# Optimization experiments

Measured on AMD Instinct MI355X. Metric: run time of the kernel, lower is better.

The kernel has to match this reference:

```python
import jax, jax.numpy as jnp
import numpy as np

MD_R = 64          # low-rank R
NMF_STEPS = 7      # EVAL_STEPS
INV_T = 1.0
EPS = 1e-6
GN_GROUPS = 32


def _nmf_step(x, bases, coef):
    # x: (B,D,N), bases: (B,D,R), coef: (B,N,R) -- multiplicative NMF updates
    btb = jnp.einsum('bdr,bdk->brk', bases, bases)                 # (B,R,R)
    coef = coef * jnp.einsum('bdn,bdr->bnr', x, bases) / (
        jnp.einsum('bnr,brk->bnk', coef, btb) + EPS)
    ctc = jnp.einsum('bnr,bnk->brk', coef, coef)                   # (B,R,R)
    bases = bases * jnp.einsum('bdn,bnr->bdr', x, coef) / (
        jnp.einsum('bdr,brk->bdk', bases, ctc) + EPS)
    return bases, coef


def setup_inputs() -> dict:
    key = jax.random.key(0)
    ks = jax.random.split(key, 7)
    B, C, H, W = 8, 256, 64, 64
    x = jax.random.normal(ks[0], (B, C, H, W), jnp.float32)
    w_in = jax.random.normal(ks[1], (C, C), jnp.float32) * 0.02
    b_in = jnp.zeros((C,), jnp.float32)
    w_out = jax.random.normal(ks[2], (C, C), jnp.float32) * 0.02
    gn_gamma = jnp.ones((C,), jnp.float32)
    gn_beta = jnp.zeros((C,), jnp.float32)
    bases_init = jax.random.uniform(ks[3], (B, C, MD_R), jnp.float32)  # RAND_INIT bases
    return {"x": x, "w_in": w_in, "b_in": b_in, "w_out": w_out,
            "gn_gamma": gn_gamma, "gn_beta": gn_beta, "bases_init": bases_init}


def reference(x, w_in, b_in, w_out, gn_gamma, gn_beta, bases_init):
    B, C, H, W = x.shape
    N = H * W
    # ham_in: 1x1 conv with bias, then relu
    h = jnp.einsum('bchw,oc->bohw', x, w_in) + b_in[None, :, None, None]
    h = jax.nn.relu(h)
    # NMF2D: flatten spatial (SPATIAL=True, S=1 -> D=C)
    xm = h.reshape(B, C, N)                                         # (B,D,N)
    # F.normalize(rand bases, dim=1)
    bases = bases_init / jnp.maximum(
        jnp.linalg.norm(bases_init, axis=1, keepdims=True), 1e-12)
    # local_inference runs under no_grad in the original; math identical here
    xs = jax.lax.stop_gradient(xm)
    coef = jax.nn.softmax(INV_T * jnp.einsum('bdn,bdr->bnr', xs, bases), axis=-1)
    for _ in range(NMF_STEPS):
        bases, coef = _nmf_step(xs, bases, coef)
    bases = jax.lax.stop_gradient(bases)
    coef = jax.lax.stop_gradient(coef)
    # compute_coef (differentiable w.r.t. xm)
    btb = jnp.einsum('bdr,bdk->brk', bases, bases)
    coef = coef * jnp.einsum('bdn,bdr->bnr', xm, bases) / (
        jnp.einsum('bnr,brk->bnk', coef, btb) + EPS)
    rec = jnp.einsum('bdr,bnr->bdn', bases, coef).reshape(B, C, H, W)
    # ham_out: 1x1 conv (no bias) + GroupNorm(32)
    o = jnp.einsum('bchw,oc->bohw', rec, w_out)
    g = o.reshape(B, GN_GROUPS, C // GN_GROUPS, H, W)
    mu = g.mean(axis=(2, 3, 4), keepdims=True)
    var = g.var(axis=(2, 3, 4), keepdims=True)
    g = (g - mu) * jax.lax.rsqrt(var + 1e-5)
    o = g.reshape(B, C, H, W) * gn_gamma[None, :, None, None] + gn_beta[None, :, None, None]
    # residual + relu
    return jax.nn.relu(x + o)
```

## Files before the change

kernel.cpp:

```cpp
#include <hip/hip_runtime.h>

#define B_ 8
#define C_ 256
#define N_ 4096
#define R_ 64
#define STEPS_ 7
#define NCH_ 128
#define NSP_ 32
#define EPS_ 1e-6f

typedef unsigned short u16;
typedef short bf8v __attribute__((ext_vector_type(8)));
typedef float f4v __attribute__((ext_vector_type(4)));

#define MFMA(a, b, c) __builtin_amdgcn_mfma_f32_16x16x32_bf16((a), (b), (c), 0, 0, 0)

__device__ __forceinline__ u16 bf(float x) {
  union { float f; unsigned u; } v; v.f = x;
  return (u16)((v.u + 0x7FFFu + ((v.u >> 16) & 1u)) >> 16);
}
__device__ __forceinline__ float bf2f(u16 x) {
  union { unsigned u; float f; } v; v.u = (unsigned)x << 16; return v.f;
}
__device__ __forceinline__ bf8v ldf(const u16* p) { return *(const bf8v*)p; }

__global__ __launch_bounds__(256)
void prep_kernel(const float* __restrict__ binit, float* __restrict__ bases,
                 u16* __restrict__ bases_bf, u16* __restrict__ basesT,
                 const float* __restrict__ w1, const float* __restrict__ w2,
                 u16* __restrict__ w1b, u16* __restrict__ w2b) {
  const int t = threadIdx.x;
  if (blockIdx.x >= 8) {
    const int i = (blockIdx.x - 8) * 256 + t;
    w1b[i] = bf(w1[i]);
    w2b[i] = bf(w2[i]);
    return;
  }
  const int b = blockIdx.x;
  const int rr = t & 63, dq = t >> 6;
  const float* src = binit + (size_t)b * C_ * R_;
  float* dst = bases + (size_t)b * C_ * R_;
  u16* dbf = bases_bf + (size_t)b * C_ * R_;
  u16* dT  = basesT + (size_t)b * R_ * C_;
  float vals[64];
  float s = 0.f;
#pragma unroll
  for (int i = 0; i < 64; ++i) {
    float v = src[(size_t)(dq + 4 * i) * R_ + rr];
    vals[i] = v; s = fmaf(v, v, s);
  }
  __shared__ float red[4][64];
  red[dq][rr] = s;
  __syncthreads();
  float nrm = fmaxf(sqrtf(red[0][rr] + red[1][rr] + red[2][rr] + red[3][rr]), 1e-12f);
  const float inv = 1.f / nrm;
#pragma unroll
  for (int i = 0; i < 64; ++i) {
    const int d = dq + 4 * i;
    const float v = vals[i] * inv;
    dst[(size_t)d * R_ + rr] = v;
    dbf[(size_t)d * R_ + rr] = bf(v);
    dT[(size_t)rr * C_ + d]  = bf(v);
  }
}

__global__ __launch_bounds__(256)
void xpose_kernel(const float* __restrict__ x, u16* __restrict__ xT) {
  const int n0 = blockIdx.x * 64, c0 = blockIdx.y * 64, b = blockIdx.z;
  __shared__ float lds[64][65];
  const int t = threadIdx.x;
  const float* xb = x + (size_t)b * C_ * N_;
  const int row = t >> 4, col4 = (t & 15) * 4;
#pragma unroll
  for (int p = 0; p < 4; ++p) {
    float4 v = *(const float4*)&xb[(size_t)(c0 + row + 16 * p) * N_ + n0 + col4];
    lds[row + 16 * p][col4 + 0] = v.x; lds[row + 16 * p][col4 + 1] = v.y;
    lds[row + 16 * p][col4 + 2] = v.z; lds[row + 16 * p][col4 + 3] = v.w;
  }
  __syncthreads();
  const int r = t >> 2, cb = (t & 3) * 16;
  __align__(16) u16 tmp[16];
#pragma unroll
  for (int j = 0; j < 16; ++j) tmp[j] = bf(lds[cb + j][r]);
  u16* o = xT + (size_t)b * N_ * C_ + (size_t)(n0 + r) * C_ + c0 + cb;
  *(uint4*)o = *(uint4*)tmp;
  *(uint4*)(o + 8) = *(uint4*)(tmp + 8);
}

template<bool CONV1>
__global__ __launch_bounds__(256)
void conv_mfma_kernel(const u16* __restrict__ A, const u16* __restrict__ W,
                      const float* __restrict__ bias, u16* __restrict__ h_dn,
                      u16* __restrict__ h_nd, float* __restrict__ of32,
                      float* __restrict__ pstats) {
  const int nb0 = blockIdx.x * 128, ob0 = blockIdx.y * 128, b = blockIdx.z;
  const int t = threadIdx.x, w = t >> 6, lane = t & 63, g = lane >> 4, c = lane & 15;
  const int n_base = nb0 + (w >> 1) * 64, o_base = ob0 + (w & 1) * 64;
  const u16* Ab = A + (size_t)b * N_ * C_;
  f4v acc[4][4] = {};
  for (int k0 = 0; k0 < C_; k0 += 32) {
    bf8v av[4], wv[4];
#pragma unroll
    for (int mi = 0; mi < 4; ++mi)
      av[mi] = ldf(Ab + (size_t)(n_base + mi * 16 + c) * C_ + k0 + g * 8);
#pragma unroll
    for (int nj = 0; nj < 4; ++nj)
      wv[nj] = ldf(W + (size_t)(o_base + nj * 16 + c) * C_ + k0 + g * 8);
#pragma unroll
    for (int mi = 0; mi < 4; ++mi)
#pragma unroll
      for (int nj = 0; nj < 4; ++nj)
        acc[mi][nj] = MFMA(av[mi], wv[nj], acc[mi][nj]);
  }
  __shared__ float lds[64][65];
  float sacc0 = 0.f, sacc1 = 0.f, s2acc0 = 0.f, s2acc1 = 0.f;
  for (int p = 0; p < 4; ++p) {
    if (w == p) {
#pragma unroll
      for (int mi = 0; mi < 4; ++mi)
#pragma unroll
        for (int nj = 0; nj < 4; ++nj) {
          const float bb = CONV1 ? bias[o_base + nj * 16 + c] : 0.f;
#pragma unroll
          for (int rg = 0; rg < 4; ++rg) {
            float v = acc[mi][nj][rg];
            if (CONV1) v = fmaxf(v + bb, 0.f);
            lds[mi * 16 + g * 4 + rg][nj * 16 + c] = v;
          }
        }
    }
    __syncthreads();
    const int pn = nb0 + (p >> 1) * 64, po = ob0 + (p & 1) * 64;
    if (CONV1) {
      {
        const int n = t >> 2, ob2 = (t & 3) * 16;
        __align__(16) u16 tmp[16];
#pragma unroll
        for (int j = 0; j < 16; ++j) tmp[j] = bf(lds[n][ob2 + j]);
        u16* o = h_nd + (size_t)b * N_ * C_ + (size_t)(pn + n) * C_ + po + ob2;
        *(uint4*)o = *(uint4*)tmp; *(uint4*)(o + 8) = *(uint4*)(tmp + 8);
      }
      {
        const int oo = t >> 2, nb2 = (t & 3) * 16;
        __align__(16) u16 tmp[16];
#pragma unroll
        for (int j = 0; j < 16; ++j) tmp[j] = bf(lds[nb2 + j][oo]);
        u16* o = h_dn + (size_t)b * C_ * N_ + (size_t)(po + oo) * N_ + pn + nb2;
        *(uint4*)o = *(uint4*)tmp; *(uint4*)(o + 8) = *(uint4*)(tmp + 8);
      }
    } else {
      const int oo = t >> 2, nb2 = (t & 3) * 16;
      float* o = of32 + (size_t)b * C_ * N_ + (size_t)(po + oo) * N_ + pn + nb2;
      float ls = 0.f, ls2 = 0.f;
#pragma unroll
      for (int q = 0; q < 4; ++q) {
        float4 v = make_float4(lds[nb2 + q * 4 + 0][oo], lds[nb2 + q * 4 + 1][oo],
                               lds[nb2 + q * 4 + 2][oo], lds[nb2 + q * 4 + 3][oo]);
        *(float4*)&o[q * 4] = v;
        ls += v.x + v.y + v.z + v.w;
        ls2 = fmaf(v.x, v.x, ls2); ls2 = fmaf(v.y, v.y, ls2);
        ls2 = fmaf(v.z, v.z, ls2); ls2 = fmaf(v.w, v.w, ls2);
      }
      if ((p & 1) == 0) { sacc0 += ls; s2acc0 += ls2; }
      else              { sacc1 += ls; s2acc1 += ls2; }
    }
    __syncthreads();
  }
  if (!CONV1) {
    const int oo = t >> 2, q4 = t & 3;
    lds[oo][q4] = sacc0;      lds[oo][4 + q4] = s2acc0;
    lds[oo][8 + q4] = sacc1;  lds[oo][12 + q4] = s2acc1;
    __syncthreads();
    if (t < 128) {
      const int hh = t >> 6, oo2 = t & 63;
      const int base = hh * 8;
      float s = lds[oo2][base] + lds[oo2][base + 1] + lds[oo2][base + 2] + lds[oo2][base + 3];
      float s2 = lds[oo2][base + 4] + lds[oo2][base + 5] + lds[oo2][base + 6] + lds[oo2][base + 7];
      float* ps = pstats + (((size_t)blockIdx.z * 32 + blockIdx.x) * 256 +
                            (size_t)blockIdx.y * 128 + hh * 64 + oo2) * 2;
      ps[0] = s; ps[1] = s2;
    }
  }
}

template<int MODE>
__global__ __launch_bounds__(512)
void nmf_kernel(const u16* __restrict__ h_nd, const u16* __restrict__ h_dn,
                const u16* __restrict__ basesT, const u16* __restrict__ bases_bf,
                u16* __restrict__ coef_bf, u16* __restrict__ rec_nd,
                float* __restrict__ ctcp, float* __restrict__ xcp) {
  const int nc0 = blockIdx.x * NCH_;
  const int b = blockIdx.y;
  const int t = threadIdx.x, w = t >> 6, lane = t & 63, g = lane >> 4, c = lane & 15;
  __shared__ u16 bT_s[64 * 256];
  __shared__ u16 btb_s[64][72];
  __shared__ u16 coef_s[128][72];
  __shared__ u16 coefT_s[64][136];
  const u16* hb = h_nd + (size_t)b * N_ * C_;
  const u16* bT = basesT + (size_t)b * R_ * C_;
  u16* cb = coef_bf + (size_t)b * N_ * R_;

#pragma unroll
  for (int i = 0; i < 4; ++i) {
    const int lin = t + i * 512;
    const int r = lin >> 5, k = lin & 31;
    *(uint4*)&bT_s[r * 256 + ((k ^ (r & 7)) * 8)] =
        *(const uint4*)&bT[(size_t)r * C_ + k * 8];
  }
  if (MODE != 0) {
    const int row = t >> 2, seg = (t & 3) * 16;
    const u16* src = cb + (size_t)(nc0 + row) * R_ + seg;
    *(uint4*)&coef_s[row][seg] = *(const uint4*)src;
    *(uint4*)&coef_s[row][seg + 8] = *(const uint4*)(src + 8);
  }
  __syncthreads();

  const int nl = w * 16 + c;

  f4v num[4] = {}, bt[4] = {};
  const u16* An = hb + (size_t)(nc0 + nl) * C_;
  for (int k0 = 0; k0 < C_; k0 += 32) {
    const int kc = (k0 >> 3) + g;
    bf8v bv[4];
#pragma unroll
    for (int nj = 0; nj < 4; ++nj)
      bv[nj] = *(const bf8v*)&bT_s[(nj * 16 + c) * 256 + ((kc ^ (c & 7)) * 8)];
    bf8v a = ldf(An + k0 + g * 8);
#pragma unroll
    for (int nj = 0; nj < 4; ++nj) num[nj] = MFMA(a, bv[nj], num[nj]);
    if (MODE != 0 && w < 4) {
      bf8v a2 = *(const bf8v*)&bT_s[(w * 16 + c) * 256 + ((kc ^ (c & 7)) * 8)];
#pragma unroll
      for (int nj = 0; nj < 4; ++nj) bt[nj] = MFMA(a2, bv[nj], bt[nj]);
    }
  }

  if (MODE == 0) {
#pragma unroll
    for (int rg = 0; rg < 4; ++rg) {
      float m = fmaxf(fmaxf(num[0][rg], num[1][rg]), fmaxf(num[2][rg], num[3][rg]));
#pragma unroll
      for (int off = 1; off < 16; off <<= 1) m = fmaxf(m, __shfl_xor(m, off));
      float e[4], s = 0.f;
#pragma unroll
      for (int nj = 0; nj < 4; ++nj) { e[nj] = __expf(num[nj][rg] - m); s += e[nj]; }
#pragma unroll
      for (int off = 1; off < 16; off <<= 1) s += __shfl_xor(s, off);
      const float inv = 1.f / s;
      const int n = nc0 + w * 16 + g * 4 + rg;
#pragma unroll
      for (int nj = 0; nj < 4; ++nj)
        cb[(size_t)n * R_ + nj * 16 + c] = bf(e[nj] * inv);
    }
    return;
  }

  if (w < 4) {
#pragma unroll
    for (int nj = 0; nj < 4; ++nj)
#pragma unroll
      for (int rg = 0; rg < 4; ++rg)
        btb_s[w * 16 + g * 4 + rg][nj * 16 + c] = bf(bt[nj][rg]);
  }
  __syncthreads();

  f4v den[4] = {};
#pragma unroll
  for (int k0 = 0; k0 < R_; k0 += 32) {
    bf8v a = *(const bf8v*)&coef_s[nl][k0 + g * 8];
#pragma unroll
    for (int nj = 0; nj < 4; ++nj)
      den[nj] = MFMA(a, *(const bf8v*)&btb_s[nj * 16 + c][k0 + g * 8], den[nj]);
  }
  __syncthreads();

#pragma unroll
  for (int nj = 0; nj < 4; ++nj)
#pragma unroll
    for (int rg = 0; rg < 4; ++rg) {
      const int row = w * 16 + g * 4 + rg, r = nj * 16 + c;
      const float old = bf2f(coef_s[row][r]);
      const u16 nv = bf(old * num[nj][rg] / (den[nj][rg] + EPS_));
      coef_s[row][r] = nv;
      if (MODE == 1) coefT_s[r][row] = nv;
    }
  __syncthreads();

  {
    const int row = t >> 2, seg = (t & 3) * 16;
    u16* dst = cb + (size_t)(nc0 + row) * R_ + seg;
    *(uint4*)dst = *(const uint4*)&coef_s[row][seg];
    *(uint4*)(dst + 8) = *(const uint4*)&coef_s[row][seg + 8];
  }

  if (MODE == 1) {
    f4v xa[2][4] = {};
    const u16* hd = h_dn + (size_t)b * C_ * N_;
    for (int k0 = 0; k0 < NCH_; k0 += 32) {
      bf8v bv[4];
#pragma unroll
      for (int nj = 0; nj < 4; ++nj)
        bv[nj] = *(const bf8v*)&coefT_s[nj * 16 + c][k0 + g * 8];
#pragma unroll
      for (int mi = 0; mi < 2; ++mi) {
        bf8v a = ldf(hd + (size_t)(w * 32 + mi * 16 + c) * N_ + nc0 + k0 + g * 8);
#pragma unroll
        for (int nj = 0; nj < 4; ++nj) xa[mi][nj] = MFMA(a, bv[nj], xa[mi][nj]);
      }
    }
    float* xo = xcp + ((size_t)b * NSP_ + blockIdx.x) * (C_ * R_);
#pragma unroll
    for (int mi = 0; mi < 2; ++mi)
#pragma unroll
      for (int nj = 0; nj < 4; ++nj)
#pragma unroll
        for (int rg = 0; rg < 4; ++rg)
          xo[(size_t)(w * 32 + mi * 16 + g * 4 + rg) * R_ + nj * 16 + c] = xa[mi][nj][rg];
    if (w < 4) {
      f4v ca[4] = {};
      for (int k0 = 0; k0 < NCH_; k0 += 32) {
        bf8v a = *(const bf8v*)&coefT_s[w * 16 + c][k0 + g * 8];
#pragma unroll
        for (int nj = 0; nj < 4; ++nj)
          ca[nj] = MFMA(a, *(const bf8v*)&coefT_s[nj * 16 + c][k0 + g * 8], ca[nj]);
      }
      float* co = ctcp + ((size_t)b * NSP_ + blockIdx.x) * (R_ * R_);
#pragma unroll
      for (int nj = 0; nj < 4; ++nj)
#pragma unroll
        for (int rg = 0; rg < 4; ++rg)
          co[(size_t)(w * 16 + g * 4 + rg) * R_ + nj * 16 + c] = ca[nj][rg];
    }
  }

  if (MODE == 2) {
    f4v ra[8][2] = {};
    const u16* Bb = bases_bf + (size_t)b * C_ * R_;
#pragma unroll
    for (int k0 = 0; k0 < R_; k0 += 32) {
      bf8v bv[2];
#pragma unroll
      for (int nj = 0; nj < 2; ++nj)
        bv[nj] = ldf(Bb + (size_t)(w * 32 + nj * 16 + c) * R_ + k0 + g * 8);
#pragma unroll
      for (int mi = 0; mi < 8; ++mi) {
        bf8v a = *(const bf8v*)&coef_s[mi * 16 + c][k0 + g * 8];
#pragma unroll
        for (int nj = 0; nj < 2; ++nj) ra[mi][nj] = MFMA(a, bv[nj], ra[mi][nj]);
      }
    }
    u16* ro = rec_nd + (size_t)b * N_ * C_;
#pragma unroll
    for (int mi = 0; mi < 8; ++mi)
#pragma unroll
      for (int nj = 0; nj < 2; ++nj)
#pragma unroll
        for (int rg = 0; rg < 4; ++rg)
          ro[(size_t)(nc0 + mi * 16 + g * 4 + rg) * C_ + w * 32 + nj * 16 + c] =
              bf(ra[mi][nj][rg]);
  }
}

__global__ __launch_bounds__(256)
void bases_update_kernel(const float* __restrict__ xcp, const float* __restrict__ ctcp,
                         float* __restrict__ bases, u16* __restrict__ bases_bf,
                         u16* __restrict__ basesT) {
  const int dt = blockIdx.x & 3, rt = blockIdx.x >> 2, b = blockIdx.y;
  const int d0 = dt * 64, rb = rt * 16;
  float* bb = bases + (size_t)b * C_ * R_;
  __shared__ float ctc_s[64][16];
  __shared__ float b_s[64][65];
  const int t = threadIdx.x;
  {
    const int k = t >> 2, cr = (t & 3) * 4;
    float4 a = make_float4(0, 0, 0, 0);
    for (int s = 0; s < NSP_; ++s) {
      float4 v = *(const float4*)&ctcp[((size_t)b * NSP_ + s) * (R_ * R_) + (size_t)k * R_ + rb + cr];
      a.x += v.x; a.y += v.y; a.z += v.z; a.w += v.w;
    }
    *(float4*)&ctc_s[k][cr] = a;
  }
  {
    const int lc = t & 63, lr = t >> 6;
#pragma unroll
    for (int p = 0; p < 16; ++p)
      b_s[lr + 4 * p][lc] = bb[(size_t)(d0 + lr + 4 * p) * R_ + lc];
  }
  __syncthreads();
  const int dd = t >> 2, r0 = rb + (t & 3) * 4, cr = (t & 3) * 4;
  float4 num2 = make_float4(0, 0, 0, 0);
  for (int s = 0; s < NSP_; ++s) {
    float4 v = *(const float4*)&xcp[(((size_t)b * NSP_ + s) * C_ + d0 + dd) * R_ + r0];
    num2.x += v.x; num2.y += v.y; num2.z += v.z; num2.w += v.w;
  }
  float4 den = make_float4(0, 0, 0, 0);
#pragma unroll
  for (int k = 0; k < 64; ++k) {
    const float a = b_s[dd][k];
    float4 cv = *(const float4*)&ctc_s[k][cr];
    den.x = fmaf(a, cv.x, den.x); den.y = fmaf(a, cv.y, den.y);
    den.z = fmaf(a, cv.z, den.z); den.w = fmaf(a, cv.w, den.w);
  }
  float4 o;
  o.x = b_s[dd][r0 + 0] * num2.x / (den.x + EPS_);
  o.y = b_s[dd][r0 + 1] * num2.y / (den.y + EPS_);
  o.z = b_s[dd][r0 + 2] * num2.z / (den.z + EPS_);
  o.w = b_s[dd][r0 + 3] * num2.w / (den.w + EPS_);
  *(float4*)&bb[(size_t)(d0 + dd) * R_ + r0] = o;
  u16* obf = bases_bf + (size_t)b * C_ * R_ + (size_t)(d0 + dd) * R_ + r0;
  obf[0] = bf(o.x); obf[1] = bf(o.y); obf[2] = bf(o.z); obf[3] = bf(o.w);
  u16* oT = basesT + (size_t)b * R_ * C_ + d0 + dd;
  oT[(size_t)(r0 + 0) * C_] = bf(o.x); oT[(size_t)(r0 + 1) * C_] = bf(o.y);
  oT[(size_t)(r0 + 2) * C_] = bf(o.z); oT[(size_t)(r0 + 3) * C_] = bf(o.w);
}

__global__ __launch_bounds__(256)
void gn_final_kernel(const float* __restrict__ x, const float* __restrict__ gamma,
                     const float* __restrict__ beta, const float* __restrict__ pstats,
                     float* __restrict__ out) {
  const int t = threadIdx.x;
  const size_t gid0 = (size_t)blockIdx.x * 256;
  const size_t idx0 = gid0 * 4;
  const int b = (int)(idx0 >> 20);
  const int c = (int)((idx0 & ((1u << 20) - 1)) >> 12);
  const int g = c >> 3;
  float s, s2;
  {
    const int nb = t >> 3, ch = g * 8 + (t & 7);
    const float* ps = pstats + (((size_t)b * 32 + nb) * 256 + ch) * 2;
    s = ps[0]; s2 = ps[1];
  }
#pragma unroll
  for (int off = 32; off > 0; off >>= 1) { s += __shfl_down(s, off); s2 += __shfl_down(s2, off); }
  __shared__ float rs[4], rs2[4], fin[2];
  if ((t & 63) == 0) { rs[t >> 6] = s; rs2[t >> 6] = s2; }
  __syncthreads();
  if (t == 0) {
    float S = rs[0] + rs[1] + rs[2] + rs[3];
    float S2 = rs2[0] + rs2[1] + rs2[2] + rs2[3];
    float mean = S / 32768.f;
    float var = S2 / 32768.f - mean * mean;
    fin[0] = mean; fin[1] = rsqrtf(var + 1e-5f);
  }
  __syncthreads();
  const float mean = fin[0], rstd = fin[1];
  const float ga = gamma[c] * rstd;
  const float be = beta[c] - mean * ga;
  const size_t gid = gid0 + t;
  float4 ov = ((const float4*)out)[gid];
  float4 xv = ((const float4*)x)[gid];
  float4 r;
  r.x = fmaxf(fmaf(ov.x, ga, be) + xv.x, 0.f);
  r.y = fmaxf(fmaf(ov.y, ga, be) + xv.y, 0.f);
  r.z = fmaxf(fmaf(ov.z, ga, be) + xv.z, 0.f);
  r.w = fmaxf(fmaf(ov.w, ga, be) + xv.w, 0.f);
  ((float4*)out)[gid] = r;
}

extern "C" void kernel_launch(void* const* d_in, const int* in_sizes, int n_in,
                              void* d_out, int out_size, void* d_ws, size_t ws_size,
                              hipStream_t stream) {
  (void)in_sizes; (void)n_in; (void)out_size; (void)ws_size;
  const float* x     = (const float*)d_in[0];
  const float* w_in  = (const float*)d_in[1];
  const float* b_in  = (const float*)d_in[2];
  const float* w_out = (const float*)d_in[3];
  const float* gamma = (const float*)d_in[4];
  const float* beta  = (const float*)d_in[5];
  const float* binit = (const float*)d_in[6];
  float* out = (float*)d_out;

  float* p = (float*)d_ws;
  u16* xT = (u16*)p;        p += 4194304;
  u16* rec_nd = xT;
  u16* h_nd = (u16*)p;      p += 4194304;
  u16* h_dn = (u16*)p;      p += 4194304;
  u16* coef_bf = (u16*)p;   p += 1048576;
  float* bases = p;         p += 131072;
  u16* bases_bf = (u16*)p;  p += 65536;
  u16* basesT = (u16*)p;    p += 65536;
  float* ctcp = p;          p += 1048576;
  float* xcp = p;           p += 4194304;
  u16* w1b = (u16*)p;       p += 32768;
  u16* w2b = (u16*)p;       p += 32768;
  float* pstats = p;        p += 131072;

  prep_kernel<<<dim3(264), 256, 0, stream>>>(binit, bases, bases_bf, basesT,
                                             w_in, w_out, w1b, w2b);
  xpose_kernel<<<dim3(64, 4, 8), 256, 0, stream>>>(x, xT);
  conv_mfma_kernel<true><<<dim3(32, 2, 8), 256, 0, stream>>>(xT, w1b, b_in, h_dn, h_nd,
                                                             nullptr, nullptr);
  nmf_kernel<0><<<dim3(32, 8), 512, 0, stream>>>(h_nd, h_dn, basesT, bases_bf, coef_bf,
                                                 nullptr, nullptr, nullptr);
  for (int it = 0; it < STEPS_; ++it) {
    nmf_kernel<1><<<dim3(32, 8), 512, 0, stream>>>(h_nd, h_dn, basesT, bases_bf, coef_bf,
                                                   nullptr, ctcp, xcp);
    bases_update_kernel<<<dim3(16, 8), 256, 0, stream>>>(xcp, ctcp, bases, bases_bf, basesT);
  }
  nmf_kernel<2><<<dim3(32, 8), 512, 0, stream>>>(h_nd, h_dn, basesT, bases_bf, coef_bf,
                                                 rec_nd, nullptr, nullptr);
  conv_mfma_kernel<false><<<dim3(32, 2, 8), 256, 0, stream>>>(rec_nd, w2b, nullptr,
                                                              nullptr, nullptr, out, pstats);
  gn_final_kernel<<<dim3((B_ * C_ * N_) / 4 / 256), 256, 0, stream>>>(x, gamma, beta,
                                                                      pstats, out);
}
```

Baseline: 287.6 us.

## Fold w_out into bases and fuse softmax init into first NMF step

Computes M2 = W_out·bases once per batch (low-rank, C×R) and runs the output conv directly on coef (K=64 instead of K=256), so the rank-R reconstruction tensor is never materialized in global memory. Also merges the softmax initialization pass into the first NMF iteration, which removes one full nmf_kernel launch and one read of h_nd. The bf16 bases copy is dropped. The reassociation changes rounding slightly because M2 is stored in bf16.

```diff
diff --git a/kernel.cpp b/kernel.cpp
--- a/kernel.cpp
+++ b/kernel.cpp
@@ -26,7 +26,7 @@
 
 __global__ __launch_bounds__(256)
 void prep_kernel(const float* __restrict__ binit, float* __restrict__ bases,
-                 u16* __restrict__ bases_bf, u16* __restrict__ basesT,
+                 u16* __restrict__ basesT,
                  const float* __restrict__ w1, const float* __restrict__ w2,
                  u16* __restrict__ w1b, u16* __restrict__ w2b) {
   const int t = threadIdx.x;
@@ -40,7 +40,6 @@
   const int rr = t & 63, dq = t >> 6;
   const float* src = binit + (size_t)b * C_ * R_;
   float* dst = bases + (size_t)b * C_ * R_;
-  u16* dbf = bases_bf + (size_t)b * C_ * R_;
   u16* dT  = basesT + (size_t)b * R_ * C_;
   float vals[64];
   float s = 0.f;
@@ -59,7 +58,6 @@
     const int d = dq + 4 * i;
     const float v = vals[i] * inv;
     dst[(size_t)d * R_ + rr] = v;
-    dbf[(size_t)d * R_ + rr] = bf(v);
     dT[(size_t)rr * C_ + d]  = bf(v);
   }
 }
@@ -87,12 +85,10 @@
   *(uint4*)(o + 8) = *(uint4*)(tmp + 8);
 }
 
-template<bool CONV1>
 __global__ __launch_bounds__(256)
-void conv_mfma_kernel(const u16* __restrict__ A, const u16* __restrict__ W,
-                      const float* __restrict__ bias, u16* __restrict__ h_dn,
-                      u16* __restrict__ h_nd, float* __restrict__ of32,
-                      float* __restrict__ pstats) {
+void conv1_kernel(const u16* __restrict__ A, const u16* __restrict__ W,
+                  const float* __restrict__ bias, u16* __restrict__ h_dn,
+                  u16* __restrict__ h_nd) {
   const int nb0 = blockIdx.x * 128, ob0 = blockIdx.y * 128, b = blockIdx.z;
   const int t = threadIdx.x, w = t >> 6, lane = t & 63, g = lane >> 4, c = lane & 15;
   const int n_base = nb0 + (w >> 1) * 64, o_base = ob0 + (w & 1) * 64;
@@ -113,60 +109,319 @@
         acc[mi][nj] = MFMA(av[mi], wv[nj], acc[mi][nj]);
   }
   __shared__ float lds[64][65];
+  for (int p = 0; p < 4; ++p) {
+    if (w == p) {
+#pragma unroll
+      for (int mi = 0; mi < 4; ++mi)
+#pragma unroll
+        for (int nj = 0; nj < 4; ++nj) {
+          const float bb = bias[o_base + nj * 16 + c];
+#pragma unroll
+          for (int rg = 0; rg < 4; ++rg)
+            lds[mi * 16 + g * 4 + rg][nj * 16 + c] = fmaxf(acc[mi][nj][rg] + bb, 0.f);
+        }
+    }
+    __syncthreads();
+    const int pn = nb0 + (p >> 1) * 64, po = ob0 + (p & 1) * 64;
+    {
+      const int n = t >> 2, ob2 = (t & 3) * 16;
+      __align__(16) u16 tmp[16];
+#pragma unroll
+      for (int j = 0; j < 16; ++j) tmp[j] = bf(lds[n][ob2 + j]);
+      u16* o = h_nd + (size_t)b * N_ * C_ + (size_t)(pn + n) * C_ + po + ob2;
+      *(uint4*)o = *(uint4*)tmp; *(uint4*)(o + 8) = *(uint4*)(tmp + 8);
+    }
+    {
+      const int oo = t >> 2, nb2 = (t & 3) * 16;
+      __align__(16) u16 tmp[16];
+#pragma unroll
+      for (int j = 0; j < 16; ++j) tmp[j] = bf(lds[nb2 + j][oo]);
+      u16* o = h_dn + (size_t)b * C_ * N_ + (size_t)(po + oo) * N_ + pn + nb2;
+      *(uint4*)o = *(uint4*)tmp; *(uint4*)(o + 8) = *(uint4*)(tmp + 8);
+    }
+    __syncthreads();
+  }
+}
+
+template<int MODE>
+__global__ __launch_bounds__(512)
+void nmf_kernel(const u16* __restrict__ h_nd, const u16* __restrict__ h_dn,
+                const u16* __restrict__ basesT, const u16* __restrict__ w2b,
+                u16* __restrict__ coef_bf, u16* __restrict__ m2_bf,
+                float* __restrict__ ctcp, float* __restrict__ xcp) {
+  const int nc0 = blockIdx.x * NCH_;
+  const int b = blockIdx.y;
+  const int t = threadIdx.x, w = t >> 6, lane = t & 63, g = lane >> 4, c = lane & 15;
+  __shared__ u16 bT_s[64 * 256];
+  __shared__ u16 btb_s[64][72];
+  __shared__ u16 coef_s[128][72];
+  __shared__ u16 coefT_s[64][136];
+  const u16* hb = h_nd + (size_t)b * N_ * C_;
+  const u16* bT = basesT + (size_t)b * R_ * C_;
+  u16* cb = coef_bf + (size_t)b * N_ * R_;
+
+#pragma unroll
+  for (int i = 0; i < 4; ++i) {
+    const int lin = t + i * 512;
+    const int r = lin >> 5, k = lin & 31;
+    *(uint4*)&bT_s[r * 256 + ((k ^ (r & 7)) * 8)] =
+        *(const uint4*)&bT[(size_t)r * C_ + k * 8];
+  }
+  if (MODE != 0) {
+    const int row = t >> 2, seg = (t & 3) * 16;
+    const u16* src = cb + (size_t)(nc0 + row) * R_ + seg;
+    *(uint4*)&coef_s[row][seg] = *(const uint4*)src;
+    *(uint4*)&coef_s[row][seg + 8] = *(const uint4*)(src + 8);
+  }
+  __syncthreads();
+
+  const int nl = w * 16 + c;
+
+  f4v num[4] = {}, bt[4] = {};
+  const u16* An = hb + (size_t)(nc0 + nl) * C_;
+  for (int k0 = 0; k0 < C_; k0 += 32) {
+    const int kc = (k0 >> 3) + g;
+    bf8v bv[4];
+#pragma unroll
+    for (int nj = 0; nj < 4; ++nj)
+      bv[nj] = *(const bf8v*)&bT_s[(nj * 16 + c) * 256 + ((kc ^ (c & 7)) * 8)];
+    bf8v a = ldf(An + k0 + g * 8);
+#pragma unroll
+    for (int nj = 0; nj < 4; ++nj) num[nj] = MFMA(a, bv[nj], num[nj]);
+    if (w < 4) {
+      bf8v a2 = *(const bf8v*)&bT_s[(w * 16 + c) * 256 + ((kc ^ (c & 7)) * 8)];
+#pragma unroll
+      for (int nj = 0; nj < 4; ++nj) bt[nj] = MFMA(a2, bv[nj], bt[nj]);
+    }
+  }
+
+  if (MODE == 0) {
+#pragma unroll
+    for (int rg = 0; rg < 4; ++rg) {
+      float m = fmaxf(fmaxf(num[0][rg], num[1][rg]), fmaxf(num[2][rg], num[3][rg]));
+#pragma unroll
+      for (int off = 1; off < 16; off <<= 1) m = fmaxf(m, __shfl_xor(m, off));
+      float e[4], s = 0.f;
+#pragma unroll
+      for (int nj = 0; nj < 4; ++nj) { e[nj] = __expf(num[nj][rg] - m); s += e[nj]; }
+#pragma unroll
+      for (int off = 1; off < 16; off <<= 1) s += __shfl_xor(s, off);
+      const float inv = 1.f / s;
+#pragma unroll
+      for (int nj = 0; nj < 4; ++nj)
+        coef_s[w * 16 + g * 4 + rg][nj * 16 + c] = bf(e[nj] * inv);
+    }
+  }
+
+  if (w < 4) {
+#pragma unroll
+    for (int nj = 0; nj < 4; ++nj)
+#pragma unroll
+      for (int rg = 0; rg < 4; ++rg)
+        btb_s[w * 16 + g * 4 + rg][nj * 16 + c] = bf(bt[nj][rg]);
+  }
+  __syncthreads();
+
+  f4v den[4] = {};
+#pragma unroll
+  for (int k0 = 0; k0 < R_; k0 += 32) {
+    bf8v a = *(const bf8v*)&coef_s[nl][k0 + g * 8];
+#pragma unroll
+    for (int nj = 0; nj < 4; ++nj)
+      den[nj] = MFMA(a, *(const bf8v*)&btb_s[nj * 16 + c][k0 + g * 8], den[nj]);
+  }
+  __syncthreads();
+
+#pragma unroll
+  for (int nj = 0; nj < 4; ++nj)
+#pragma unroll
+    for (int rg = 0; rg < 4; ++rg) {
+      const int row = w * 16 + g * 4 + rg, r = nj * 16 + c;
+      const float old = bf2f(coef_s[row][r]);
+      const u16 nv = bf(old * num[nj][rg] / (den[nj][rg] + EPS_));
+      coef_s[row][r] = nv;
+      if (MODE <= 1) coefT_s[r][row] = nv;
+    }
+  __syncthreads();
+
+  {
+    const int row = t >> 2, seg = (t & 3) * 16;
+    u16* dst = cb + (size_t)(nc0 + row) * R_ + seg;
+    *(uint4*)dst = *(const uint4*)&coef_s[row][seg];
+    *(uint4*)(dst + 8) = *(const uint4*)&coef_s[row][seg + 8];
+  }
+
+  if (MODE <= 1) {
+    f4v xa[2][4] = {};
+    const u16* hd = h_dn + (size_t)b * C_ * N_;
+    for (int k0 = 0; k0 < NCH_; k0 += 32) {
+      bf8v bv[4];
+#pragma unroll
+      for (int nj = 0; nj < 4; ++nj)
+        bv[nj] = *(const bf8v*)&coefT_s[nj * 16 + c][k0 + g * 8];
+#pragma unroll
+      for (int mi = 0; mi < 2; ++mi) {
+        bf8v a = ldf(hd + (size_t)(w * 32 + mi * 16 + c) * N_ + nc0 + k0 + g * 8);
+#pragma unroll
+        for (int nj = 0; nj < 4; ++nj) xa[mi][nj] = MFMA(a, bv[nj], xa[mi][nj]);
+      }
+    }
+    float* xo = xcp + ((size_t)b * NSP_ + blockIdx.x) * (C_ * R_);
+#pragma unroll
+    for (int mi = 0; mi < 2; ++mi)
+#pragma unroll
+      for (int nj = 0; nj < 4; ++nj)
+#pragma unroll
+        for (int rg = 0; rg < 4; ++rg)
+          xo[(size_t)(w * 32 + mi * 16 + g * 4 + rg) * R_ + nj * 16 + c] = xa[mi][nj][rg];
+    if (w < 4) {
+      f4v ca[4] = {};
+      for (int k0 = 0; k0 < NCH_; k0 += 32) {
+        bf8v a = *(const bf8v*)&coefT_s[w * 16 + c][k0 + g * 8];
+#pragma unroll
+        for (int nj = 0; nj < 4; ++nj)
+          ca[nj] = MFMA(a, *(const bf8v*)&coefT_s[nj * 16 + c][k0 + g * 8], ca[nj]);
+      }
+      float* co = ctcp + ((size_t)b * NSP_ + blockIdx.x) * (R_ * R_);
+#pragma unroll
+      for (int nj = 0; nj < 4; ++nj)
+#pragma unroll
+        for (int rg = 0; rg < 4; ++rg)
+          co[(size_t)(w * 16 + g * 4 + rg) * R_ + nj * 16 + c] = ca[nj][rg];
+    }
+  }
+
+  if (MODE == 2 && blockIdx.x == 0) {
+    f4v ma[2][4] = {};
+    for (int k0 = 0; k0 < C_; k0 += 32) {
+      const int kc = (k0 >> 3) + g;
+      bf8v bv[4];
+#pragma unroll
+      for (int nj = 0; nj < 4; ++nj)
+        bv[nj] = *(const bf8v*)&bT_s[(nj * 16 + c) * 256 + ((kc ^ (c & 7)) * 8)];
+#pragma unroll
+      for (int mi = 0; mi < 2; ++mi) {
+        bf8v a = ldf(w2b + (size_t)(w * 32 + mi * 16 + c) * C_ + k0 + g * 8);
+#pragma unroll
+        for (int nj = 0; nj < 4; ++nj) ma[mi][nj] = MFMA(a, bv[nj], ma[mi][nj]);
+      }
+    }
+    u16* mo = m2_bf + (size_t)b * C_ * R_;
+#pragma unroll
+    for (int mi = 0; mi < 2; ++mi)
+#pragma unroll
+      for (int nj = 0; nj < 4; ++nj)
+#pragma unroll
+        for (int rg = 0; rg < 4; ++rg)
+          mo[(size_t)(w * 32 + mi * 16 + g * 4 + rg) * R_ + nj * 16 + c] = bf(ma[mi][nj][rg]);
+  }
+}
+
+__global__ __launch_bounds__(256)
+void bases_update_kernel(const float* __restrict__ xcp, const float* __restrict__ ctcp,
+                         float* __restrict__ bases, u16* __restrict__ basesT) {
+  const int dt = blockIdx.x & 3, rt = blockIdx.x >> 2, b = blockIdx.y;
+  const int d0 = dt * 64, rb = rt * 16;
+  float* bb = bases + (size_t)b * C_ * R_;
+  __shared__ float ctc_s[64][16];
+  __shared__ float b_s[64][65];
+  const int t = threadIdx.x;
+  {
+    const int k = t >> 2, cr = (t & 3) * 4;
+    float4 a = make_float4(0, 0, 0, 0);
+    for (int s = 0; s < NSP_; ++s) {
+      float4 v = *(const float4*)&ctcp[((size_t)b * NSP_ + s) * (R_ * R_) + (size_t)k * R_ + rb + cr];
+      a.x += v.x; a.y += v.y; a.z += v.z; a.w += v.w;
+    }
+    *(float4*)&ctc_s[k][cr] = a;
+  }
+  {
+    const int lc = t & 63, lr = t >> 6;
+#pragma unroll
+    for (int p = 0; p < 16; ++p)
+      b_s[lr + 4 * p][lc] = bb[(size_t)(d0 + lr + 4 * p) * R_ + lc];
+  }
+  __syncthreads();
+  const int dd = t >> 2, r0 = rb + (t & 3) * 4, cr = (t & 3) * 4;
+  float4 num2 = make_float4(0, 0, 0, 0);
+  for (int s = 0; s < NSP_; ++s) {
+    float4 v = *(const float4*)&xcp[(((size_t)b * NSP_ + s) * C_ + d0 + dd) * R_ + r0];
+    num2.x += v.x; num2.y += v.y; num2.z += v.z; num2.w += v.w;
+  }
+  float4 den = make_float4(0, 0, 0, 0);
+#pragma unroll
+  for (int k = 0; k < 64; ++k) {
+    const float a = b_s[dd][k];
+    float4 cv = *(const float4*)&ctc_s[k][cr];
+    den.x = fmaf(a, cv.x, den.x); den.y = fmaf(a, cv.y, den.y);
+    den.z = fmaf(a, cv.z, den.z); den.w = fmaf(a, cv.w, den.w);
+  }
+  float4 o;
+  o.x = b_s[dd][r0 + 0] * num2.x / (den.x + EPS_);
+  o.y = b_s[dd][r0 + 1] * num2.y / (den.y + EPS_);
+  o.z = b_s[dd][r0 + 2] * num2.z / (den.z + EPS_);
+  o.w = b_s[dd][r0 + 3] * num2.w / (den.w + EPS_);
+  *(float4*)&bb[(size_t)(d0 + dd) * R_ + r0] = o;
+  u16* oT = basesT + (size_t)b * R_ * C_ + d0 + dd;
+  oT[(size_t)(r0 + 0) * C_] = bf(o.x); oT[(size_t)(r0 + 1) * C_] = bf(o.y);
+  oT[(size_t)(r0 + 2) * C_] = bf(o.z); oT[(size_t)(r0 + 3) * C_] = bf(o.w);
+}
+
+__global__ __launch_bounds__(256)
+void conv2_kernel(const u16* __restrict__ coef, const u16* __restrict__ m2,
+                  float* __restrict__ of32, float* __restrict__ pstats) {
+  const int nb0 = blockIdx.x * 128, ob0 = blockIdx.y * 128, b = blockIdx.z;
+  const int t = threadIdx.x, w = t >> 6, lane = t & 63, g = lane >> 4, c = lane & 15;
+  const int n_base = nb0 + (w >> 1) * 64, o_base = ob0 + (w & 1) * 64;
+  const u16* Ab = coef + (size_t)b * N_ * R_;
+  const u16* Wb = m2 + (size_t)b * C_ * R_;
+  f4v acc[4][4] = {};
+#pragma unroll
+  for (int k0 = 0; k0 < R_; k0 += 32) {
+    bf8v av[4], wv[4];
+#pragma unroll
+    for (int mi = 0; mi < 4; ++mi)
+      av[mi] = ldf(Ab + (size_t)(n_base + mi * 16 + c) * R_ + k0 + g * 8);
+#pragma unroll
+    for (int nj = 0; nj < 4; ++nj)
+      wv[nj] = ldf(Wb + (size_t)(o_base + nj * 16 + c) * R_ + k0 + g * 8);
+#pragma unroll
+    for (int mi = 0; mi < 4; ++mi)
+#pragma unroll
+      for (int nj = 0; nj < 4; ++nj)
+        acc[mi][nj] = MFMA(av[mi], wv[nj], acc[mi][nj]);
+  }
+  __shared__ float lds[64][65];
   float sacc0 = 0.f, sacc1 = 0.f, s2acc0 = 0.f, s2acc1 = 0.f;
   for (int p = 0; p < 4; ++p) {
     if (w == p) {
 #pragma unroll
       for (int mi = 0; mi < 4; ++mi)
 #pragma unroll
-        for (int nj = 0; nj < 4; ++nj) {
-          const float bb = CONV1 ? bias[o_base + nj * 16 + c] : 0.f;
-#pragma unroll
-          for (int rg = 0; rg < 4; ++rg) {
-            float v = acc[mi][nj][rg];
-            if (CONV1) v = fmaxf(v + bb, 0.f);
-            lds[mi * 16 + g * 4 + rg][nj * 16 + c] = v;
-          }
-        }
+        for (int nj = 0; nj < 4; ++nj)
+#pragma unroll
+          for (int rg = 0; rg < 4; ++rg)
+            lds[mi * 16 + g * 4 + rg][nj * 16 + c] = acc[mi][nj][rg];
     }
     __syncthreads();
     const int pn = nb0 + (p >> 1) * 64, po = ob0 + (p & 1) * 64;
-    if (CONV1) {
-      {
-        const int n = t >> 2, ob2 = (t & 3) * 16;
-        __align__(16) u16 tmp[16];
-#pragma unroll
-        for (int j = 0; j < 16; ++j) tmp[j] = bf(lds[n][ob2 + j]);
-        u16* o = h_nd + (size_t)b * N_ * C_ + (size_t)(pn + n) * C_ + po + ob2;
-        *(uint4*)o = *(uint4*)tmp; *(uint4*)(o + 8) = *(uint4*)(tmp + 8);
-      }
-      {
-        const int oo = t >> 2, nb2 = (t & 3) * 16;
-        __align__(16) u16 tmp[16];
-#pragma unroll
-        for (int j = 0; j < 16; ++j) tmp[j] = bf(lds[nb2 + j][oo]);
-        u16* o = h_dn + (size_t)b * C_ * N_ + (size_t)(po + oo) * N_ + pn + nb2;
-        *(uint4*)o = *(uint4*)tmp; *(uint4*)(o + 8) = *(uint4*)(tmp + 8);
-      }
-    } else {
-      const int oo = t >> 2, nb2 = (t & 3) * 16;
-      float* o = of32 + (size_t)b * C_ * N_ + (size_t)(po + oo) * N_ + pn + nb2;
-      float ls = 0.f, ls2 = 0.f;
-#pragma unroll
-      for (int q = 0; q < 4; ++q) {
-        float4 v = make_float4(lds[nb2 + q * 4 + 0][oo], lds[nb2 + q * 4 + 1][oo],
-                               lds[nb2 + q * 4 + 2][oo], lds[nb2 + q * 4 + 3][oo]);
-        *(float4*)&o[q * 4] = v;
-        ls += v.x + v.y + v.z + v.w;
-        ls2 = fmaf(v.x, v.x, ls2); ls2 = fmaf(v.y, v.y, ls2);
-        ls2 = fmaf(v.z, v.z, ls2); ls2 = fmaf(v.w, v.w, ls2);
-      }
-      if ((p & 1) == 0) { sacc0 += ls; s2acc0 += ls2; }
-      else              { sacc1 += ls; s2acc1 += ls2; }
-    }
+    const int oo = t >> 2, nb2 = (t & 3) * 16;
+    float* o = of32 + (size_t)b * C_ * N_ + (size_t)(po + oo) * N_ + pn + nb2;
+    float ls = 0.f, ls2 = 0.f;
+#pragma unroll
+    for (int q = 0; q < 4; ++q) {
+      float4 v = make_float4(lds[nb2 + q * 4 + 0][oo], lds[nb2 + q * 4 + 1][oo],
+                             lds[nb2 + q * 4 + 2][oo], lds[nb2 + q * 4 + 3][oo]);
+      *(float4*)&o[q * 4] = v;
+      ls += v.x + v.y + v.z + v.w;
+      ls2 = fmaf(v.x, v.x, ls2); ls2 = fmaf(v.y, v.y, ls2);
+      ls2 = fmaf(v.z, v.z, ls2); ls2 = fmaf(v.w, v.w, ls2);
+    }
+    if ((p & 1) == 0) { sacc0 += ls; s2acc0 += ls2; }
+    else              { sacc1 += ls; s2acc1 += ls2; }
     __syncthreads();
   }
-  if (!CONV1) {
+  {
     const int oo = t >> 2, q4 = t & 3;
     lds[oo][q4] = sacc0;      lds[oo][4 + q4] = s2acc0;
     lds[oo][8 + q4] = sacc1;  lds[oo][12 + q4] = s2acc1;
@@ -181,237 +436,6 @@
       ps[0] = s; ps[1] = s2;
     }
   }
-}
-
-template<int MODE>
-__global__ __launch_bounds__(512)
-void nmf_kernel(const u16* __restrict__ h_nd, const u16* __restrict__ h_dn,
-                const u16* __restrict__ basesT, const u16* __restrict__ bases_bf,
-                u16* __restrict__ coef_bf, u16* __restrict__ rec_nd,
-                float* __restrict__ ctcp, float* __restrict__ xcp) {
-  const int nc0 = blockIdx.x * NCH_;
-  const int b = blockIdx.y;
-  const int t = threadIdx.x, w = t >> 6, lane = t & 63, g = lane >> 4, c = lane & 15;
-  __shared__ u16 bT_s[64 * 256];
-  __shared__ u16 btb_s[64][72];
-  __shared__ u16 coef_s[128][72];
-  __shared__ u16 coefT_s[64][136];
-  const u16* hb = h_nd + (size_t)b * N_ * C_;
-  const u16* bT = basesT + (size_t)b * R_ * C_;
-  u16* cb = coef_bf + (size_t)b * N_ * R_;
-
-#pragma unroll
-  for (int i = 0; i < 4; ++i) {
-    const int lin = t + i * 512;
-    const int r = lin >> 5, k = lin & 31;
-    *(uint4*)&bT_s[r * 256 + ((k ^ (r & 7)) * 8)] =
-        *(const uint4*)&bT[(size_t)r * C_ + k * 8];
-  }
-  if (MODE != 0) {
-    const int row = t >> 2, seg = (t & 3) * 16;
-    const u16* src = cb + (size_t)(nc0 + row) * R_ + seg;
-    *(uint4*)&coef_s[row][seg] = *(const uint4*)src;
-    *(uint4*)&coef_s[row][seg + 8] = *(const uint4*)(src + 8);
-  }
-  __syncthreads();
-
-  const int nl = w * 16 + c;
-
-  f4v num[4] = {}, bt[4] = {};
-  const u16* An = hb + (size_t)(nc0 + nl) * C_;
-  for (int k0 = 0; k0 < C_; k0 += 32) {
-    const int kc = (k0 >> 3) + g;
-    bf8v bv[4];
-#pragma unroll
-    for (int nj = 0; nj < 4; ++nj)
-      bv[nj] = *(const bf8v*)&bT_s[(nj * 16 + c) * 256 + ((kc ^ (c & 7)) * 8)];
-    bf8v a = ldf(An + k0 + g * 8);
-#pragma unroll
-    for (int nj = 0; nj < 4; ++nj) num[nj] = MFMA(a, bv[nj], num[nj]);
-    if (MODE != 0 && w < 4) {
-      bf8v a2 = *(const bf8v*)&bT_s[(w * 16 + c) * 256 + ((kc ^ (c & 7)) * 8)];
-#pragma unroll
-      for (int nj = 0; nj < 4; ++nj) bt[nj] = MFMA(a2, bv[nj], bt[nj]);
-    }
-  }
-
-  if (MODE == 0) {
-#pragma unroll
-    for (int rg = 0; rg < 4; ++rg) {
-      float m = fmaxf(fmaxf(num[0][rg], num[1][rg]), fmaxf(num[2][rg], num[3][rg]));
-#pragma unroll
-      for (int off = 1; off < 16; off <<= 1) m = fmaxf(m, __shfl_xor(m, off));
-      float e[4], s = 0.f;
-#pragma unroll
-      for (int nj = 0; nj < 4; ++nj) { e[nj] = __expf(num[nj][rg] - m); s += e[nj]; }
-#pragma unroll
-      for (int off = 1; off < 16; off <<= 1) s += __shfl_xor(s, off);
-      const float inv = 1.f / s;
-      const int n = nc0 + w * 16 + g * 4 + rg;
-#pragma unroll
-      for (int nj = 0; nj < 4; ++nj)
-        cb[(size_t)n * R_ + nj * 16 + c] = bf(e[nj] * inv);
-    }
-    return;
-  }
-
-  if (w < 4) {
-#pragma unroll
-    for (int nj = 0; nj < 4; ++nj)
-#pragma unroll
-      for (int rg = 0; rg < 4; ++rg)
-        btb_s[w * 16 + g * 4 + rg][nj * 16 + c] = bf(bt[nj][rg]);
-  }
-  __syncthreads();
-
-  f4v den[4] = {};
-#pragma unroll
-  for (int k0 = 0; k0 < R_; k0 += 32) {
-    bf8v a = *(const bf8v*)&coef_s[nl][k0 + g * 8];
-#pragma unroll
-    for (int nj = 0; nj < 4; ++nj)
-      den[nj] = MFMA(a, *(const bf8v*)&btb_s[nj * 16 + c][k0 + g * 8], den[nj]);
-  }
-  __syncthreads();
-
-#pragma unroll
-  for (int nj = 0; nj < 4; ++nj)
-#pragma unroll
-    for (int rg = 0; rg < 4; ++rg) {
-      const int row = w * 16 + g * 4 + rg, r = nj * 16 + c;
-      const float old = bf2f(coef_s[row][r]);
-      const u16 nv = bf(old * num[nj][rg] / (den[nj][rg] + EPS_));
-      coef_s[row][r] = nv;
-      if (MODE == 1) coefT_s[r][row] = nv;
-    }
-  __syncthreads();
-
-  {
-    const int row = t >> 2, seg = (t & 3) * 16;
-    u16* dst = cb + (size_t)(nc0 + row) * R_ + seg;
-    *(uint4*)dst = *(const uint4*)&coef_s[row][seg];
-    *(uint4*)(dst + 8) = *(const uint4*)&coef_s[row][seg + 8];
-  }
-
-  if (MODE == 1) {
-    f4v xa[2][4] = {};
-    const u16* hd = h_dn + (size_t)b * C_ * N_;
-    for (int k0 = 0; k0 < NCH_; k0 += 32) {
-      bf8v bv[4];
-#pragma unroll
-      for (int nj = 0; nj < 4; ++nj)
-        bv[nj] = *(const bf8v*)&coefT_s[nj * 16 + c][k0 + g * 8];
-#pragma unroll
-      for (int mi = 0; mi < 2; ++mi) {
-        bf8v a = ldf(hd + (size_t)(w * 32 + mi * 16 + c) * N_ + nc0 + k0 + g * 8);
-#pragma unroll
-        for (int nj = 0; nj < 4; ++nj) xa[mi][nj] = MFMA(a, bv[nj], xa[mi][nj]);
-      }
-    }
-    float* xo = xcp + ((size_t)b * NSP_ + blockIdx.x) * (C_ * R_);
-#pragma unroll
-    for (int mi = 0; mi < 2; ++mi)
-#pragma unroll
-      for (int nj = 0; nj < 4; ++nj)
-#pragma unroll
-        for (int rg = 0; rg < 4; ++rg)
-          xo[(size_t)(w * 32 + mi * 16 + g * 4 + rg) * R_ + nj * 16 + c] = xa[mi][nj][rg];
-    if (w < 4) {
-      f4v ca[4] = {};
-      for (int k0 = 0; k0 < NCH_; k0 += 32) {
-        bf8v a = *(const bf8v*)&coefT_s[w * 16 + c][k0 + g * 8];
-#pragma unroll
-        for (int nj = 0; nj < 4; ++nj)
-          ca[nj] = MFMA(a, *(const bf8v*)&coefT_s[nj * 16 + c][k0 + g * 8], ca[nj]);
-      }
-      float* co = ctcp + ((size_t)b * NSP_ + blockIdx.x) * (R_ * R_);
-#pragma unroll
-      for (int nj = 0; nj < 4; ++nj)
-#pragma unroll
-        for (int rg = 0; rg < 4; ++rg)
-          co[(size_t)(w * 16 + g * 4 + rg) * R_ + nj * 16 + c] = ca[nj][rg];
-    }
-  }
-
-  if (MODE == 2) {
-    f4v ra[8][2] = {};
-    const u16* Bb = bases_bf + (size_t)b * C_ * R_;
-#pragma unroll
-    for (int k0 = 0; k0 < R_; k0 += 32) {
-      bf8v bv[2];
-#pragma unroll
-      for (int nj = 0; nj < 2; ++nj)
-        bv[nj] = ldf(Bb + (size_t)(w * 32 + nj * 16 + c) * R_ + k0 + g * 8);
-#pragma unroll
-      for (int mi = 0; mi < 8; ++mi) {
-        bf8v a = *(const bf8v*)&coef_s[mi * 16 + c][k0 + g * 8];
-#pragma unroll
-        for (int nj = 0; nj < 2; ++nj) ra[mi][nj] = MFMA(a, bv[nj], ra[mi][nj]);
-      }
-    }
-    u16* ro = rec_nd + (size_t)b * N_ * C_;
-#pragma unroll
-    for (int mi = 0; mi < 8; ++mi)
-#pragma unroll
-      for (int nj = 0; nj < 2; ++nj)
-#pragma unroll
-        for (int rg = 0; rg < 4; ++rg)
-          ro[(size_t)(nc0 + mi * 16 + g * 4 + rg) * C_ + w * 32 + nj * 16 + c] =
-              bf(ra[mi][nj][rg]);
-  }
-}
-
-__global__ __launch_bounds__(256)
-void bases_update_kernel(const float* __restrict__ xcp, const float* __restrict__ ctcp,
-                         float* __restrict__ bases, u16* __restrict__ bases_bf,
-                         u16* __restrict__ basesT) {
-  const int dt = blockIdx.x & 3, rt = blockIdx.x >> 2, b = blockIdx.y;
-  const int d0 = dt * 64, rb = rt * 16;
-  float* bb = bases + (size_t)b * C_ * R_;
-  __shared__ float ctc_s[64][16];
-  __shared__ float b_s[64][65];
-  const int t = threadIdx.x;
-  {
-    const int k = t >> 2, cr = (t & 3) * 4;
-    float4 a = make_float4(0, 0, 0, 0);
-    for (int s = 0; s < NSP_; ++s) {
-      float4 v = *(const float4*)&ctcp[((size_t)b * NSP_ + s) * (R_ * R_) + (size_t)k * R_ + rb + cr];
-      a.x += v.x; a.y += v.y; a.z += v.z; a.w += v.w;
-    }
-    *(float4*)&ctc_s[k][cr] = a;
-  }
-  {
-    const int lc = t & 63, lr = t >> 6;
-#pragma unroll
-    for (int p = 0; p < 16; ++p)
-      b_s[lr + 4 * p][lc] = bb[(size_t)(d0 + lr + 4 * p) * R_ + lc];
-  }
-  __syncthreads();
-  const int dd = t >> 2, r0 = rb + (t & 3) * 4, cr = (t & 3) * 4;
-  float4 num2 = make_float4(0, 0, 0, 0);
-  for (int s = 0; s < NSP_; ++s) {
-    float4 v = *(const float4*)&xcp[(((size_t)b * NSP_ + s) * C_ + d0 + dd) * R_ + r0];
-    num2.x += v.x; num2.y += v.y; num2.z += v.z; num2.w += v.w;
-  }
-  float4 den = make_float4(0, 0, 0, 0);
-#pragma unroll
-  for (int k = 0; k < 64; ++k) {
-    const float a = b_s[dd][k];
-    float4 cv = *(const float4*)&ctc_s[k][cr];
-    den.x = fmaf(a, cv.x, den.x); den.y = fmaf(a, cv.y, den.y);
-    den.z = fmaf(a, cv.z, den.z); den.w = fmaf(a, cv.w, den.w);
-  }
-  float4 o;
-  o.x = b_s[dd][r0 + 0] * num2.x / (den.x + EPS_);
-  o.y = b_s[dd][r0 + 1] * num2.y / (den.y + EPS_);
-  o.z = b_s[dd][r0 + 2] * num2.z / (den.z + EPS_);
-  o.w = b_s[dd][r0 + 3] * num2.w / (den.w + EPS_);
-  *(float4*)&bb[(size_t)(d0 + dd) * R_ + r0] = o;
-  u16* obf = bases_bf + (size_t)b * C_ * R_ + (size_t)(d0 + dd) * R_ + r0;
-  obf[0] = bf(o.x); obf[1] = bf(o.y); obf[2] = bf(o.z); obf[3] = bf(o.w);
-  u16* oT = basesT + (size_t)b * R_ * C_ + d0 + dd;
-  oT[(size_t)(r0 + 0) * C_] = bf(o.x); oT[(size_t)(r0 + 1) * C_] = bf(o.y);
-  oT[(size_t)(r0 + 2) * C_] = bf(o.z); oT[(size_t)(r0 + 3) * C_] = bf(o.w);
 }
 
 __global__ __launch_bounds__(256)
@@ -472,35 +496,33 @@
 
   float* p = (float*)d_ws;
   u16* xT = (u16*)p;        p += 4194304;
-  u16* rec_nd = xT;
   u16* h_nd = (u16*)p;      p += 4194304;
   u16* h_dn = (u16*)p;      p += 4194304;
   u16* coef_bf = (u16*)p;   p += 1048576;
   float* bases = p;         p += 131072;
-  u16* bases_bf = (u16*)p;  p += 65536;
   u16* basesT = (u16*)p;    p += 65536;
+  u16* m2_bf = (u16*)p;     p += 65536;
   float* ctcp = p;          p += 1048576;
   float* xcp = p;           p += 4194304;
   u16* w1b = (u16*)p;       p += 32768;
   u16* w2b = (u16*)p;       p += 32768;
   float* pstats = p;        p += 131072;
 
-  prep_kernel<<<dim3(264), 256, 0, stream>>>(binit, bases, bases_bf, basesT,
-                                             w_in, w_out, w1b, w2b);
+  prep_kernel<<<dim3(264), 256, 0, stream>>>(binit, bases, basesT, w_in, w_out, w1b, w2b);
   xpose_kernel<<<dim3(64, 4, 8), 256, 0, stream>>>(x, xT);
-  conv_mfma_kernel<true><<<dim3(32, 2, 8), 256, 0, stream>>>(xT, w1b, b_in, h_dn, h_nd,
-                                                             nullptr, nullptr);
-  nmf_kernel<0><<<dim3(32, 8), 512, 0, stream>>>(h_nd, h_dn, basesT, bases_bf, coef_bf,
-                                                 nullptr, nullptr, nullptr);
-  for (int it = 0; it < STEPS_; ++it) {
-    nmf_kernel<1><<<dim3(32, 8), 512, 0, stream>>>(h_nd, h_dn, basesT, bases_bf, coef_bf,
-                                                   nullptr, ctcp, xcp);
-    bases_update_kernel<<<dim3(16, 8), 256, 0, stream>>>(xcp, ctcp, bases, bases_bf, basesT);
-  }
-  nmf_kernel<2><<<dim3(32, 8), 512, 0, stream>>>(h_nd, h_dn, basesT, bases_bf, coef_bf,
-                                                 rec_nd, nullptr, nullptr);
-  conv_mfma_kernel<false><<<dim3(32, 2, 8), 256, 0, stream>>>(rec_nd, w2b, nullptr,
-                                                              nullptr, nullptr, out, pstats);
+  conv1_kernel<<<dim3(32, 2, 8), 256, 0, stream>>>(xT, w1b, b_in, h_dn, h_nd);
+
+  nmf_kernel<0><<<dim3(32, 8), 512, 0, stream>>>(h_nd, h_dn, basesT, w2b, coef_bf,
+                                                 m2_bf, ctcp, xcp);
+  bases_update_kernel<<<dim3(16, 8), 256, 0, stream>>>(xcp, ctcp, bases, basesT);
+  for (int it = 1; it < STEPS_; ++it) {
+    nmf_kernel<1><<<dim3(32, 8), 512, 0, stream>>>(h_nd, h_dn, basesT, w2b, coef_bf,
+                                                   m2_bf, ctcp, xcp);
+    bases_update_kernel<<<dim3(16, 8), 256, 0, stream>>>(xcp, ctcp, bases, basesT);
+  }
+  nmf_kernel<2><<<dim3(32, 8), 512, 0, stream>>>(h_nd, h_dn, basesT, w2b, coef_bf,
+                                                 m2_bf, ctcp, xcp);
+  conv2_kernel<<<dim3(32, 2, 8), 256, 0, stream>>>(coef_bf, m2_bf, out, pstats);
   gn_final_kernel<<<dim3((B_ * C_ * N_) / 4 / 256), 256, 0, stream>>>(x, gamma, beta,
                                                                       pstats, out);
 }
```

After: 272.0 us. 5.4% less time.
